# Kernel optimization log

Measured on AMD Instinct MI355X. Metric: run time of the kernel, lower is better.

## Reference

```python
import jax, jax.numpy as jnp
import numpy as np

N_NODES = 100000
F_DIM = 256
NNZ = 1600000  # ~avg degree 16 incidence pairs


def setup_inputs() -> dict:
    key = jax.random.key(0)
    k0, k1, k2, k3 = jax.random.split(key, 4)
    x = jax.random.normal(k0, (N_NODES, F_DIM), dtype=jnp.float32)
    edge_index = jax.random.randint(k1, (2, NNZ), 0, N_NODES, dtype=jnp.int32)
    scale = (2.0 / F_DIM) ** 0.5  # kaiming_normal
    W1 = jax.random.normal(k2, (F_DIM, F_DIM), dtype=jnp.float32) * scale
    W2 = jax.random.normal(k3, (F_DIM, F_DIM), dtype=jnp.float32) * scale
    b1 = jnp.zeros((F_DIM,), jnp.float32)
    b2 = jnp.zeros((F_DIM,), jnp.float32)
    a = jnp.full((1,), 0.25, jnp.float32)  # PReLU shared weight
    return {"x": x, "edge_index": edge_index, "W1": W1, "b1": b1,
            "W2": W2, "b2": b2, "a": a}


def _prelu(x, a):
    return jnp.where(x >= 0, x, a * x)


def _hconv(x, W, b, src, dst, n):
    # PyG HypergraphConv (use_attention=False, edge_weight=1):
    # X' = D^{-1} H B^{-1} H^T X Theta + bias
    xt = x @ W                                   # [N, F]
    ones = jnp.ones(src.shape, xt.dtype)
    D = jax.ops.segment_sum(ones, src, num_segments=n)   # node degree
    B = jax.ops.segment_sum(ones, dst, num_segments=n)   # hyperedge degree
    Dinv = jnp.where(D > 0, 1.0 / D, 0.0)
    Binv = jnp.where(B > 0, 1.0 / B, 0.0)
    # node -> hyperedge: m_e = B^{-1}_e * sum_{i in e} xt_i
    m = jax.ops.segment_sum(xt[src], dst, num_segments=n) * Binv[:, None]
    # hyperedge -> node: out_i = D^{-1}_i * sum_{e ni i} m_e
    out = jax.ops.segment_sum(m[dst], src, num_segments=n) * Dinv[:, None]
    return out + b


def reference(x, edge_index, W1, b1, W2, b2, a):
    src, dst = edge_index[0], edge_index[1]
    n = x.shape[0]  # hyperedge ids are node ids in this module
    h = _prelu(_hconv(x, W1, b1, src, dst, n), a)
    h = _hconv(h, W2, b2, src, dst, n) + x  # residual
    return _prelu(h, a)
```

## Files before the change

### kernel.cpp

```cpp
#include <hip/hip_runtime.h>
#include <hip/hip_bf16.h>


#define F_DIM 256
#define CAP 48
#define BW_SHIFT 9
#define CHUNK 2048

using bf16x8 = __attribute__((ext_vector_type(8))) short;
using f32x4  = __attribute__((ext_vector_type(4))) float;
using half4  = __attribute__((ext_vector_type(4))) _Float16;

__device__ __forceinline__ short f2bf(float f) {
    __hip_bfloat16 h = __float2bfloat16(f);
    return *reinterpret_cast<short*>(&h);
}
__device__ __forceinline__ float bf2f(short s) {
    return __uint_as_float(((unsigned)(unsigned short)s) << 16);
}

__global__ void init_cur_kernel(int* __restrict__ cur, int n, int buckcap) {
    int i = blockIdx.x * blockDim.x + threadIdx.x;
    if (i < n) cur[i] = i * buckcap;
}

__global__ __launch_bounds__(256) void partition_kernel(
    const int* __restrict__ src, const int* __restrict__ dst,
    int2* __restrict__ part, int* __restrict__ cur,
    int nnz, int nb, int buckcap)
{
    __shared__ int lhist[256];
    __shared__ int lscan[256];
    __shared__ int gbase[256];
    __shared__ int sh_total;
    __shared__ int2 lstage[CHUNK];

    const int tid = threadIdx.x;
    const int dir = blockIdx.y;
    const int base = blockIdx.x * CHUNK;
    const int* __restrict__ key = dir ? dst : src;
    const int* __restrict__ val = dir ? src : dst;

    lhist[tid] = 0;
    __syncthreads();

    int mykey[8], myval[8], myb[8], myr[8];
#pragma unroll
    for (int i = 0; i < 8; ++i) {
        int g = base + tid + i * 256;
        myb[i] = -1;
        if (g < nnz) {
            mykey[i] = key[g];
            myval[i] = val[g];
            myb[i] = mykey[i] >> BW_SHIFT;
            myr[i] = atomicAdd(&lhist[myb[i]], 1);
        }
    }
    __syncthreads();

    int v0 = lhist[tid];
    lscan[tid] = v0;
    __syncthreads();
    for (int off = 1; off < 256; off <<= 1) {
        int add = (tid >= off) ? lscan[tid - off] : 0;
        __syncthreads();
        lscan[tid] += add;
        __syncthreads();
    }
    int incl = lscan[tid];
    if (tid == 255) sh_total = incl;
    if (tid < nb && v0 > 0) gbase[tid] = atomicAdd(&cur[dir * nb + tid], v0);
    __syncthreads();
    lscan[tid] = incl - v0;
    __syncthreads();

#pragma unroll
    for (int i = 0; i < 8; ++i)
        if (myb[i] >= 0)
            lstage[lscan[myb[i]] + myr[i]] = make_int2(mykey[i], myval[i]);
    __syncthreads();

    const int total = sh_total;
    for (int k = tid; k < total; k += 256) {
        int2 v = lstage[k];
        int b = v.x >> BW_SHIFT;
        int pos = gbase[b] + (k - lscan[b]);
        if (pos < (dir * nb + b + 1) * buckcap)
            part[pos] = v;
    }
}

__global__ __launch_bounds__(256) void bucket_fill_kernel(
    const int2* __restrict__ part, const int* __restrict__ cur,
    int* __restrict__ adjS, int* __restrict__ adjD,
    int* __restrict__ degS, int* __restrict__ degD,
    float* __restrict__ Dinv, float* __restrict__ Binv,
    int M, int nb, int buckcap)
{
    __shared__ int lcnt[512];
    const int tid = threadIdx.x;
    const int b = blockIdx.x;
    const int dir = blockIdx.y;
    const int c = dir * nb + b;
    int* __restrict__ adj = dir ? adjD : adjS;
    int* __restrict__ deg = dir ? degD : degS;
    float* __restrict__ inv = dir ? Binv : Dinv;

    lcnt[tid] = 0;
    lcnt[tid + 256] = 0;
    __syncthreads();

    const int pbase = c * buckcap;
    const int cnt = min(cur[c] - pbase, buckcap);
    const int node0 = b << BW_SHIFT;
    for (int i = tid; i < cnt; i += 256) {
        int2 v = part[pbase + i];
        int r = atomicAdd(&lcnt[v.x - node0], 1);
        if (r < CAP) adj[(size_t)v.x * CAP + r] = v.y;
    }
    __syncthreads();
    for (int i = tid; i < 512; i += 256) {
        int node = node0 + i;
        if (node < M) {
            int d = min(lcnt[i], CAP);
            deg[node] = d;
            inv[node] = d > 0 ? 1.f / (float)d : 0.f;
        }
    }
}

__global__ void prepack_w_kernel(const float* __restrict__ W,
                                 short* __restrict__ Whi, short* __restrict__ Wlo) {
    int lane = threadIdx.x;
    int nt = blockIdx.x;
    int kt = blockIdx.y;
    int col = nt * 16 + (lane & 15);
    int krow = kt * 32 + (lane >> 4) * 8;
    size_t o = ((size_t)(kt * 16 + nt) * 64 + lane) * 8;
#pragma unroll
    for (int j = 0; j < 8; ++j) {
        float w = W[(size_t)(krow + j) * 256 + col];
        short hi = f2bf(w);
        Whi[o + j] = hi;
        Wlo[o + j] = f2bf(w - bf2f(hi));
    }
}

__global__ __launch_bounds__(256) void gemm_mfma_split(const float* __restrict__ A,
                                                       const short* __restrict__ Whi,
                                                       const short* __restrict__ Wlo,
                                                       _Float16* __restrict__ C, int M) {
    __shared__ short AsHi[4][128][8];
    __shared__ short AsLo[4][128][8];
    const int tid = threadIdx.x;
    const int w = tid >> 6, lane = tid & 63;
    const int quad = lane >> 4, l16 = lane & 15;
    const int bm = blockIdx.x * 128;
    const int bn_t = blockIdx.y * 8;
    const int wm = (w & 1) * 64;
    const int wnt = (w >> 1) * 4;

    f32x4 acc[4][4] = {};

    for (int kt = 0; kt < 8; ++kt) {
        __syncthreads();
#pragma unroll
        for (int i = 0; i < 2; ++i) {
            int idx = tid + i * 256;
            int row = idx >> 2, seg = idx & 3;
            int grow = bm + row; if (grow >= M) grow = M - 1;
            const float* ap = A + (size_t)grow * 256 + kt * 32 + seg * 8;
            float4 v0 = *(const float4*)ap;
            float4 v1 = *(const float4*)(ap + 4);
            float vv[8] = {v0.x, v0.y, v0.z, v0.w, v1.x, v1.y, v1.z, v1.w};
            union { short s[8]; int4 q; } uh, ul;
#pragma unroll
            for (int e = 0; e < 8; ++e) {
                short hi = f2bf(vv[e]);
                uh.s[e] = hi;
                ul.s[e] = f2bf(vv[e] - bf2f(hi));
            }
            *(int4*)&AsHi[seg][row][0] = uh.q;
            *(int4*)&AsLo[seg][row][0] = ul.q;
        }
        __syncthreads();

        bf16x8 ahi[4], alo[4];
#pragma unroll
        for (int i = 0; i < 4; ++i) {
            ahi[i] = *(const bf16x8*)&AsHi[quad][wm + i * 16 + l16][0];
            alo[i] = *(const bf16x8*)&AsLo[quad][wm + i * 16 + l16][0];
        }

#pragma unroll
        for (int j = 0; j < 4; ++j) {
            int nt = bn_t + wnt + j;
            size_t off = ((size_t)(kt * 16 + nt) * 64 + lane) * 8;
            bf16x8 bhi = *(const bf16x8*)(Whi + off);
            bf16x8 blo = *(const bf16x8*)(Wlo + off);
#pragma unroll
            for (int i = 0; i < 4; ++i) {
                acc[i][j] = __builtin_amdgcn_mfma_f32_16x16x32_bf16(ahi[i], bhi, acc[i][j], 0, 0, 0);
                acc[i][j] = __builtin_amdgcn_mfma_f32_16x16x32_bf16(ahi[i], blo, acc[i][j], 0, 0, 0);
                acc[i][j] = __builtin_amdgcn_mfma_f32_16x16x32_bf16(alo[i], bhi, acc[i][j], 0, 0, 0);
            }
        }
    }

#pragma unroll
    for (int i = 0; i < 4; ++i) {
#pragma unroll
        for (int j = 0; j < 4; ++j) {
            int col = (bn_t + wnt + j) * 16 + l16;
            int row0 = bm + wm + i * 16 + quad * 4;
#pragma unroll
            for (int r = 0; r < 4; ++r) {
                int row = row0 + r;
                if (row < M) C[(size_t)row * 256 + col] = (_Float16)acc[i][j][r];
            }
        }
    }
}

template <int OUT_F16>
__global__ __launch_bounds__(256) void gather_rows_kernel(const _Float16* __restrict__ src_mat,
                                                          void* __restrict__ out_mat,
                                                          const int* __restrict__ deg,
                                                          const int* __restrict__ adj,
                                                          const float* __restrict__ scale,
                                                          const float* __restrict__ bias,
                                                          const float* __restrict__ residual,
                                                          const float* __restrict__ alpha_p,
                                                          int n) {
    int wid = (blockIdx.x * blockDim.x + threadIdx.x) >> 6;
    int lane = threadIdx.x & 63;
    if (wid >= n) return;
    const int dcount = deg[wid];
    const int* arow = adj + (size_t)wid * CAP;
    int myidx = (lane < dcount) ? __builtin_nontemporal_load(arow + lane) : 0;

    const size_t lo = (size_t)lane * 4;
    float a0 = 0.f, a1 = 0.f, a2 = 0.f, a3 = 0.f;

    for (int j = 0; j < dcount; ++j) {
        int idx = __shfl(myidx, j);
        half4 v = *(const half4*)(src_mat + (size_t)idx * F_DIM + lo);
        a0 += (float)v.x; a1 += (float)v.y; a2 += (float)v.z; a3 += (float)v.w;
    }

    float sc = scale[wid];
    a0 *= sc; a1 *= sc; a2 *= sc; a3 *= sc;
    if (bias) {
        float4 bb = ((const float4*)bias)[lane];
        a0 += bb.x; a1 += bb.y; a2 += bb.z; a3 += bb.w;
    }
    if (residual) {
        const float* rp = residual + (size_t)wid * F_DIM + lo;
        float4 xv;
        xv.x = __builtin_nontemporal_load(rp + 0);
        xv.y = __builtin_nontemporal_load(rp + 1);
        xv.z = __builtin_nontemporal_load(rp + 2);
        xv.w = __builtin_nontemporal_load(rp + 3);
        a0 += xv.x; a1 += xv.y; a2 += xv.z; a3 += xv.w;
    }
    if (alpha_p) {
        float al = alpha_p[0];
        a0 = a0 >= 0.f ? a0 : al * a0;
        a1 = a1 >= 0.f ? a1 : al * a1;
        a2 = a2 >= 0.f ? a2 : al * a2;
        a3 = a3 >= 0.f ? a3 : al * a3;
    }
    if (OUT_F16) {
        half4 o;
        o.x = (_Float16)a0; o.y = (_Float16)a1; o.z = (_Float16)a2; o.w = (_Float16)a3;
        *(half4*)((_Float16*)out_mat + (size_t)wid * F_DIM + lo) = o;
    } else {
        float4 o = make_float4(a0, a1, a2, a3);
        *(float4*)((float*)out_mat + (size_t)wid * F_DIM + lo) = o;
    }
}

extern "C" void kernel_launch(void* const* d_in, const int* in_sizes, int n_in,
                              void* d_out, int out_size, void* d_ws, size_t ws_size,
                              hipStream_t stream) {
    const float* x   = (const float*)d_in[0];
    const int*   ei  = (const int*)d_in[1];
    const float* W1  = (const float*)d_in[2];
    const float* b1  = (const float*)d_in[3];
    const float* W2  = (const float*)d_in[4];
    const float* b2  = (const float*)d_in[5];
    const float* a   = (const float*)d_in[6];
    float* out = (float*)d_out;

    const int M   = in_sizes[0] / F_DIM;
    const int nnz = in_sizes[1] / 2;
    const int* src = ei;
    const int* dst = ei + nnz;

    const int NB = (M + (1 << BW_SHIFT) - 1) >> BW_SHIFT;
    const int avg = (int)(((long long)nnz << BW_SHIFT) / M);
    const int BUCKCAP = avg + avg / 8 + 256;
    const int nchunks = (nnz + CHUNK - 1) / CHUNK;

    char* p = (char*)d_ws;
    const size_t nbuf   = (size_t)M * F_DIM * sizeof(float);
    const size_t nbuf16 = (size_t)M * F_DIM * sizeof(_Float16);
    const size_t wpk    = 8 * 16 * 64 * 8 * sizeof(short);
    float*    bufH  = (float*)p;           p += nbuf;
    _Float16* bufXT = (_Float16*)p;        p += nbuf16;
    _Float16* bufM  = (_Float16*)p;        p += nbuf16;
    short* W1hi = (short*)p;               p += wpk;
    short* W1lo = (short*)p;               p += wpk;
    short* W2hi = (short*)p;               p += wpk;
    short* W2lo = (short*)p;               p += wpk;
    int* adjS   = (int*)p;                 p += (size_t)M * CAP * 4;
    int* adjD   = (int*)p;                 p += (size_t)M * CAP * 4;
    int* degS   = (int*)p;                 p += (size_t)M * 4;
    int* degD   = (int*)p;                 p += (size_t)M * 4;
    float* Dinv = (float*)p;               p += (size_t)M * 4;
    float* Binv = (float*)p;               p += (size_t)M * 4;
    int* bucketCur = (int*)p;              p += ((size_t)2 * NB * 4 + 15) & ~15ull;

    int2* part = (int2*)bufH;

    const dim3 blk(256);
    const dim3 gemm_grid((M + 127) / 128, 2);
    const int gather_blocks = (M + 3) / 4;

    init_cur_kernel<<<(2 * NB + 255) / 256, blk, 0, stream>>>(bucketCur, 2 * NB, BUCKCAP);
    partition_kernel<<<dim3(nchunks, 2), blk, 0, stream>>>(src, dst, part, bucketCur,
                                                           nnz, NB, BUCKCAP);
    bucket_fill_kernel<<<dim3(NB, 2), blk, 0, stream>>>(part, bucketCur, adjS, adjD,
                                                        degS, degD, Dinv, Binv,
                                                        M, NB, BUCKCAP);

    prepack_w_kernel<<<dim3(16, 8), 64, 0, stream>>>(W1, W1hi, W1lo);
    prepack_w_kernel<<<dim3(16, 8), 64, 0, stream>>>(W2, W2hi, W2lo);

    gemm_mfma_split<<<gemm_grid, blk, 0, stream>>>(x, W1hi, W1lo, bufXT, M);
    gather_rows_kernel<1><<<gather_blocks, blk, 0, stream>>>(bufXT, bufM, degD, adjD,
                                                             Binv, nullptr, nullptr, nullptr, M);
    gather_rows_kernel<0><<<gather_blocks, blk, 0, stream>>>(bufM, bufH, degS, adjS,
                                                             Dinv, b1, nullptr, a, M);
    gemm_mfma_split<<<gemm_grid, blk, 0, stream>>>(bufH, W2hi, W2lo, bufXT, M);
    gather_rows_kernel<1><<<gather_blocks, blk, 0, stream>>>(bufXT, bufM, degD, adjD,
                                                             Binv, nullptr, nullptr, nullptr, M);
    gather_rows_kernel<0><<<gather_blocks, blk, 0, stream>>>(bufM, out, degS, adjS,
                                                             Dinv, b2, x, a, M);
}
```

Measured before the change: 916.1 us.

## Pack partition entries into 32-bit words and widen GEMM tile to full N

Partition entries are packed into one 32-bit word holding the value shifted left by 9 and the key's low 9 bits, replacing an int2. This halves the partition buffer traffic and the shared staging space. The scatter loop now finds each element's bucket by binary search over the scan array, adding ALU work per element. Separately, the GEMM drops the two-way N split so each block computes all 256 columns with twice the accumulators per wave. That converts A to bf16 hi/lo once instead of twice, at the cost of more registers under launch_bounds(256,2).

```diff
diff --git a/kernel.cpp b/kernel.cpp
--- a/kernel.cpp
+++ b/kernel.cpp
@@ -26,14 +26,14 @@
 
 __global__ __launch_bounds__(256) void partition_kernel(
     const int* __restrict__ src, const int* __restrict__ dst,
-    int2* __restrict__ part, int* __restrict__ cur,
+    unsigned* __restrict__ part, int* __restrict__ cur,
     int nnz, int nb, int buckcap)
 {
     __shared__ int lhist[256];
     __shared__ int lscan[256];
     __shared__ int gbase[256];
     __shared__ int sh_total;
-    __shared__ int2 lstage[CHUNK];
+    __shared__ unsigned lstage[CHUNK];
 
     const int tid = threadIdx.x;
     const int dir = blockIdx.y;
@@ -44,15 +44,16 @@
     lhist[tid] = 0;
     __syncthreads();
 
-    int mykey[8], myval[8], myb[8], myr[8];
+    int myb[8], myr[8];
+    unsigned mye[8];
 #pragma unroll
     for (int i = 0; i < 8; ++i) {
         int g = base + tid + i * 256;
         myb[i] = -1;
         if (g < nnz) {
-            mykey[i] = key[g];
-            myval[i] = val[g];
-            myb[i] = mykey[i] >> BW_SHIFT;
+            int k = key[g];
+            mye[i] = ((unsigned)val[g] << 9) | (unsigned)(k & 511);
+            myb[i] = k >> BW_SHIFT;
             myr[i] = atomicAdd(&lhist[myb[i]], 1);
         }
     }
@@ -77,21 +78,26 @@
 #pragma unroll
     for (int i = 0; i < 8; ++i)
         if (myb[i] >= 0)
-            lstage[lscan[myb[i]] + myr[i]] = make_int2(mykey[i], myval[i]);
+            lstage[lscan[myb[i]] + myr[i]] = (mye[i] & ~0u) | 0u,
+            lstage[lscan[myb[i]] + myr[i]] = mye[i];
     __syncthreads();
 
     const int total = sh_total;
     for (int k = tid; k < total; k += 256) {
-        int2 v = lstage[k];
-        int b = v.x >> BW_SHIFT;
+        int lo = 0, hi = 255;
+        while (lo < hi) {
+            int mid = (lo + hi + 1) >> 1;
+            if (lscan[mid] <= k) lo = mid; else hi = mid - 1;
+        }
+        int b = lo;
         int pos = gbase[b] + (k - lscan[b]);
         if (pos < (dir * nb + b + 1) * buckcap)
-            part[pos] = v;
+            part[pos] = lstage[k];
     }
 }
 
 __global__ __launch_bounds__(256) void bucket_fill_kernel(
-    const int2* __restrict__ part, const int* __restrict__ cur,
+    const unsigned* __restrict__ part, const int* __restrict__ cur,
     int* __restrict__ adjS, int* __restrict__ adjD,
     int* __restrict__ degS, int* __restrict__ degD,
     float* __restrict__ Dinv, float* __restrict__ Binv,
@@ -114,9 +120,11 @@
     const int cnt = min(cur[c] - pbase, buckcap);
     const int node0 = b << BW_SHIFT;
     for (int i = tid; i < cnt; i += 256) {
-        int2 v = part[pbase + i];
-        int r = atomicAdd(&lcnt[v.x - node0], 1);
-        if (r < CAP) adj[(size_t)v.x * CAP + r] = v.y;
+        unsigned e = part[pbase + i];
+        int klocal = (int)(e & 511u);
+        int v = (int)(e >> 9);
+        int r = atomicAdd(&lcnt[klocal], 1);
+        if (r < CAP) adj[(size_t)(node0 + klocal) * CAP + r] = v;
     }
     __syncthreads();
     for (int i = tid; i < 512; i += 256) {
@@ -146,21 +154,20 @@
     }
 }
 
-__global__ __launch_bounds__(256) void gemm_mfma_split(const float* __restrict__ A,
-                                                       const short* __restrict__ Whi,
-                                                       const short* __restrict__ Wlo,
-                                                       _Float16* __restrict__ C, int M) {
+__global__ __launch_bounds__(256, 2) void gemm_mfma_split(const float* __restrict__ A,
+                                                          const short* __restrict__ Whi,
+                                                          const short* __restrict__ Wlo,
+                                                          _Float16* __restrict__ C, int M) {
     __shared__ short AsHi[4][128][8];
     __shared__ short AsLo[4][128][8];
     const int tid = threadIdx.x;
     const int w = tid >> 6, lane = tid & 63;
     const int quad = lane >> 4, l16 = lane & 15;
     const int bm = blockIdx.x * 128;
-    const int bn_t = blockIdx.y * 8;
     const int wm = (w & 1) * 64;
-    const int wnt = (w >> 1) * 4;
-
-    f32x4 acc[4][4] = {};
+    const int wnt = (w >> 1) * 8;
+
+    f32x4 acc[4][8] = {};
 
     for (int kt = 0; kt < 8; ++kt) {
         __syncthreads();
@@ -193,8 +200,8 @@
         }
 
 #pragma unroll
-        for (int j = 0; j < 4; ++j) {
-            int nt = bn_t + wnt + j;
+        for (int j = 0; j < 8; ++j) {
+            int nt = wnt + j;
             size_t off = ((size_t)(kt * 16 + nt) * 64 + lane) * 8;
             bf16x8 bhi = *(const bf16x8*)(Whi + off);
             bf16x8 blo = *(const bf16x8*)(Wlo + off);
@@ -210,8 +217,8 @@
 #pragma unroll
     for (int i = 0; i < 4; ++i) {
 #pragma unroll
-        for (int j = 0; j < 4; ++j) {
-            int col = (bn_t + wnt + j) * 16 + l16;
+        for (int j = 0; j < 8; ++j) {
+            int col = (wnt + j) * 16 + l16;
             int row0 = bm + wm + i * 16 + quad * 4;
 #pragma unroll
             for (int r = 0; r < 4; ++r) {
@@ -321,10 +328,10 @@
     float* Binv = (float*)p;               p += (size_t)M * 4;
     int* bucketCur = (int*)p;              p += ((size_t)2 * NB * 4 + 15) & ~15ull;
 
-    int2* part = (int2*)bufH;
+    unsigned* part = (unsigned*)bufH;
 
     const dim3 blk(256);
-    const dim3 gemm_grid((M + 127) / 128, 2);
+    const dim3 gemm_grid((M + 127) / 128);
     const int gather_blocks = (M + 3) / 4;
 
     init_cur_kernel<<<(2 * NB + 255) / 256, blk, 0, stream>>>(bucketCur, 2 * NB, BUCKCAP);
```

New measurement: 917.0 us. About the same (+0.1%).
